# Kernel tuning notes

Measured on AMD Instinct MI355X. Metric: run time of the kernel, lower is better.

Reference implementation:

```python
import jax, jax.numpy as jnp
import numpy as np

N = 100000   # nodes
E = 1600000  # edges (avg degree 16)
D = 64       # hidden_dim == in_channels
EPS = 1e-15  # PyG DGI epsilon


def gcn_conv(x, W, b, row, col, n):
    h = x @ W                                                    # [n, D]
    deg = jax.ops.segment_sum(jnp.ones(row.shape[0], x.dtype), col,
                              num_segments=n) + 1.0              # +1 for self-loop
    dis = jax.lax.rsqrt(deg)                                     # deg^-1/2
    norm = dis[row] * dis[col]                                   # [E]
    agg = jax.ops.segment_sum(h[row] * norm[:, None], col, num_segments=n)
    return agg + h * (dis * dis)[:, None] + b                    # self-loop term + bias


def encode(x, row, col, W1, b1, W2, b2, n):
    h = jax.nn.relu(gcn_conv(x, W1, b1, row, col, n))
    return gcn_conv(h, W2, b2, row, col, n)


def setup_inputs() -> dict:
    key = jax.random.key(0)
    k = jax.random.split(key, 8)
    s = 1.0 / np.sqrt(D)
    return {
        "x": jax.random.normal(k[0], (N, D), jnp.float32),
        "W1": jax.random.uniform(k[1], (D, D), jnp.float32, -s, s),
        "b1": jnp.zeros((D,), jnp.float32),
        "W2": jax.random.uniform(k[2], (D, D), jnp.float32, -s, s),
        "b2": jnp.zeros((D,), jnp.float32),
        "W_dgi": jax.random.uniform(k[3], (D, D), jnp.float32, -s, s),
        "edge_index": jax.random.randint(k[4], (2, E), 0, N, jnp.int32),
        "perm": jax.random.permutation(k[5], N).astype(jnp.int32),
    }


def reference(x, W1, b1, W2, b2, W_dgi, edge_index, perm):
    row, col = edge_index[0], edge_index[1]
    pos_z = encode(x, row, col, W1, b1, W2, b2, N)          # [N, D]
    neg_z = encode(x[perm], row, col, W1, b1, W2, b2, N)    # corrupted features, same graph
    summary = jax.nn.sigmoid(pos_z.mean(axis=0))            # [D]
    ws = W_dgi @ summary                                    # [D]
    pos_p = jax.nn.sigmoid(pos_z @ ws)                      # [N]
    neg_p = jax.nn.sigmoid(neg_z @ ws)                      # [N]
    pos_loss = -jnp.log(pos_p + EPS).mean()
    neg_loss = -jnp.log(1.0 - neg_p + EPS).mean()
    return pos_loss + neg_loss
```

## Files before the change

kernel.cpp:

```cpp
#include <hip/hip_runtime.h>
#include <hip/hip_bf16.h>
#include <math.h>

#define GG 2048
#define RB 32
#define NB_SHIFT 9
#define NPB 512
#define BINCAP 10240
#define BINREGION 12288
#define PCHUNK 2048

typedef __hip_bfloat16 bf16;
typedef unsigned int uint;
typedef unsigned short ushort;
typedef unsigned char uchar;
typedef short bf16x8 __attribute__((ext_vector_type(8)));
typedef float f32x4 __attribute__((ext_vector_type(4)));
typedef float f32x2 __attribute__((ext_vector_type(2)));

__device__ __forceinline__ bf16  f2b(float x) { return __float2bfloat16(x); }
__device__ __forceinline__ short f2bs(float x) {
    bf16 b = __float2bfloat16(x);
    return *reinterpret_cast<short*>(&b);
}
__device__ __forceinline__ ushort packfp8(float p, float n) {
    return (ushort)__builtin_amdgcn_cvt_pk_fp8_f32(p, n, 0, false);
}
__device__ __forceinline__ f32x2 unpackfp8(uint u) {
    return __builtin_amdgcn_cvt_pk_f32_fp8((int)u, false);
}
__device__ __forceinline__ f32x2 unpackfp8_hi(uint u) {
    return __builtin_amdgcn_cvt_pk_f32_fp8((int)u, true);
}

__global__ void zero_kernel(int* __restrict__ bincnt, float* __restrict__ lossacc,
                            int nb) {
    int i = threadIdx.x;
    if (i < nb) bincnt[i] = 0;
    if (i < 2)  lossacc[i] = 0.f;
}

__global__ __launch_bounds__(256) void partition_edges(
        const int* __restrict__ row, const int* __restrict__ col,
        uint* __restrict__ bins, int* __restrict__ bincnt, int E, int nb) {
    __shared__ int lcnt[256];
    __shared__ int lbase[256];
    for (int chunk = blockIdx.x * PCHUNK; chunk < E; chunk += gridDim.x * PCHUNK) {
        int end = chunk + PCHUNK < E ? chunk + PCHUNK : E;
        if (threadIdx.x < nb) lcnt[threadIdx.x] = 0;
        __syncthreads();
        for (int e = chunk + threadIdx.x; e < end; e += 256)
            atomicAdd(&lcnt[col[e] >> NB_SHIFT], 1);
        __syncthreads();
        if (threadIdx.x < nb) {
            lbase[threadIdx.x] = atomicAdd(&bincnt[threadIdx.x], lcnt[threadIdx.x]);
            lcnt[threadIdx.x] = 0;
        }
        __syncthreads();
        for (int e = chunk + threadIdx.x; e < end; e += 256) {
            int c = col[e], r = row[e];
            int g = c >> NB_SHIFT;
            int dst = lbase[g] + atomicAdd(&lcnt[g], 1);
            if (dst < BINCAP)
                bins[(size_t)g * BINCAP + dst] = ((uint)r << NB_SHIFT) | (uint)(c & (NPB - 1));
        }
        __syncthreads();
    }
}

__global__ __launch_bounds__(256) void place_lds(
        const uint* __restrict__ bins, const int* __restrict__ bincnt,
        int* __restrict__ bucket, int* __restrict__ off, int* __restrict__ cnt,
        int N) {
    __shared__ int lcnt[NPB];
    __shared__ int s[NPB];
    __shared__ int win[BINREGION];
    int b  = blockIdx.x;
    int lo = b << NB_SHIFT;
    int base = b * BINREGION;
    int ne = bincnt[b];
    if (ne > BINCAP) ne = BINCAP;
    const uint* be = bins + (size_t)b * BINCAP;
    for (int i = threadIdx.x; i < NPB; i += 256) lcnt[i] = 0;
    __syncthreads();
    for (int i = threadIdx.x; i < ne; i += 256)
        atomicAdd(&lcnt[be[i] & (NPB - 1)], 1);
    __syncthreads();
    int i0 = threadIdx.x, i1 = threadIdx.x + 256;
    s[i0] = (lcnt[i0] + 3) & ~3;
    s[i1] = (lcnt[i1] + 3) & ~3;
    __syncthreads();
    for (int st = 1; st < NPB; st <<= 1) {
        int v0 = i0 >= st ? s[i0 - st] : 0;
        int v1 = i1 >= st ? s[i1 - st] : 0;
        __syncthreads();
        s[i0] += v0; s[i1] += v1;
        __syncthreads();
    }
    for (int i = threadIdx.x; i < NPB; i += 256) {
        int v = lo + i;
        int pc = (lcnt[i] + 3) & ~3;
        int start = s[i] - pc;
        if (v < N) { off[v] = base + start; cnt[v] = lcnt[i]; }
        lcnt[i] = start;
    }
    __syncthreads();
    for (int i = threadIdx.x; i < ne; i += 256) {
        uint u = be[i];
        int slot = atomicAdd(&lcnt[u & (NPB - 1)], 1);
        if (slot < BINREGION) win[slot] = (int)(u >> NB_SHIFT);
    }
    __syncthreads();
    int wsize = s[NPB - 1];
    if (wsize > BINREGION) wsize = BINREGION;
    for (int i = threadIdx.x * 4; i < wsize; i += 1024)
        *(int4*)&bucket[base + i] = *(const int4*)&win[i];
}

__global__ __launch_bounds__(256) void gemm1_mfma(
        const float* __restrict__ X, const float* __restrict__ W,
        const int* __restrict__ perm, const int* __restrict__ cnt,
        ushort* __restrict__ out, int n) {
    int lane = threadIdx.x & 63, wid = threadIdx.x >> 6;
    int l15 = lane & 15, lg = lane >> 4;
    bf16x8 bfr[2][4];
#pragma unroll
    for (int kt = 0; kt < 2; kt++)
#pragma unroll
        for (int nt = 0; nt < 4; nt++)
#pragma unroll
            for (int i = 0; i < 8; i++)
                bfr[kt][nt][i] = f2bs(W[(kt * 32 + lg * 8 + i) * 64 + nt * 16 + l15]);
    int ntiles = (n + 15) >> 4;
    for (int t = blockIdx.x * 4 + wid; t < ntiles; t += gridDim.x * 4) {
        int rowA = t * 16 + l15;
        if (rowA >= n) rowA = n - 1;
        int prow = perm[rowA];
        const float4* xp = (const float4*)(X + (size_t)rowA * 64);
        const float4* xn = (const float4*)(X + (size_t)prow * 64);
        bf16x8 ap[2], an[2];
#pragma unroll
        for (int kt = 0; kt < 2; kt++) {
            float4 p0 = xp[kt * 8 + lg * 2], p1 = xp[kt * 8 + lg * 2 + 1];
            float4 n0 = xn[kt * 8 + lg * 2], n1 = xn[kt * 8 + lg * 2 + 1];
            ap[kt][0] = f2bs(p0.x); ap[kt][1] = f2bs(p0.y);
            ap[kt][2] = f2bs(p0.z); ap[kt][3] = f2bs(p0.w);
            ap[kt][4] = f2bs(p1.x); ap[kt][5] = f2bs(p1.y);
            ap[kt][6] = f2bs(p1.z); ap[kt][7] = f2bs(p1.w);
            an[kt][0] = f2bs(n0.x); an[kt][1] = f2bs(n0.y);
            an[kt][2] = f2bs(n0.z); an[kt][3] = f2bs(n0.w);
            an[kt][4] = f2bs(n1.x); an[kt][5] = f2bs(n1.y);
            an[kt][6] = f2bs(n1.z); an[kt][7] = f2bs(n1.w);
        }
        f32x4 accp[4], accn[4];
#pragma unroll
        for (int nt = 0; nt < 4; nt++) { accp[nt] = (f32x4)0.f; accn[nt] = (f32x4)0.f; }
#pragma unroll
        for (int nt = 0; nt < 4; nt++) {
            accp[nt] = __builtin_amdgcn_mfma_f32_16x16x32_bf16(ap[0], bfr[0][nt], accp[nt], 0, 0, 0);
            accp[nt] = __builtin_amdgcn_mfma_f32_16x16x32_bf16(ap[1], bfr[1][nt], accp[nt], 0, 0, 0);
            accn[nt] = __builtin_amdgcn_mfma_f32_16x16x32_bf16(an[0], bfr[0][nt], accn[nt], 0, 0, 0);
            accn[nt] = __builtin_amdgcn_mfma_f32_16x16x32_bf16(an[1], bfr[1][nt], accn[nt], 0, 0, 0);
        }
        float dvr[4];
#pragma unroll
        for (int reg = 0; reg < 4; reg++) {
            int node = t * 16 + lg * 4 + reg;
            dvr[reg] = node < n ? rsqrtf((float)cnt[node] + 1.0f) : 0.f;
        }
#pragma unroll
        for (int nt = 0; nt < 4; nt++)
#pragma unroll
            for (int reg = 0; reg < 4; reg++) {
                int node = t * 16 + lg * 4 + reg;
                if (node < n)
                    out[(size_t)node * 64 + nt * 16 + l15] =
                        packfp8(accp[nt][reg] * dvr[reg], accn[nt][reg] * dvr[reg]);
            }
    }
}

__global__ __launch_bounds__(256) void gemm2_mfma(
        const ushort* __restrict__ H, const float* __restrict__ W,
        const int* __restrict__ cnt, ushort* __restrict__ out, int n) {
    int lane = threadIdx.x & 63, wid = threadIdx.x >> 6;
    int l15 = lane & 15, lg = lane >> 4;
    bf16x8 bfr[2][4];
#pragma unroll
    for (int kt = 0; kt < 2; kt++)
#pragma unroll
        for (int nt = 0; nt < 4; nt++)
#pragma unroll
            for (int i = 0; i < 8; i++)
                bfr[kt][nt][i] = f2bs(W[(kt * 32 + lg * 8 + i) * 64 + nt * 16 + l15]);
    int ntiles = (n + 15) >> 4;
    for (int t = blockIdx.x * 4 + wid; t < ntiles; t += gridDim.x * 4) {
        int rowA = t * 16 + l15;
        if (rowA >= n) rowA = n - 1;
        const uint4* h = (const uint4*)(H + (size_t)rowA * 64);
        bf16x8 ap[2], an[2];
#pragma unroll
        for (int kt = 0; kt < 2; kt++) {
            uint4 hh = h[kt * 4 + lg];
            uint uu[4] = {hh.x, hh.y, hh.z, hh.w};
#pragma unroll
            for (int j = 0; j < 4; j++) {
                f32x2 lo = unpackfp8(uu[j]);
                f32x2 hi = unpackfp8_hi(uu[j]);
                ap[kt][2 * j]     = f2bs(lo.x); an[kt][2 * j]     = f2bs(lo.y);
                ap[kt][2 * j + 1] = f2bs(hi.x); an[kt][2 * j + 1] = f2bs(hi.y);
            }
        }
        f32x4 accp[4], accn[4];
#pragma unroll
        for (int nt = 0; nt < 4; nt++) { accp[nt] = (f32x4)0.f; accn[nt] = (f32x4)0.f; }
#pragma unroll
        for (int nt = 0; nt < 4; nt++) {
            accp[nt] = __builtin_amdgcn_mfma_f32_16x16x32_bf16(ap[0], bfr[0][nt], accp[nt], 0, 0, 0);
            accp[nt] = __builtin_amdgcn_mfma_f32_16x16x32_bf16(ap[1], bfr[1][nt], accp[nt], 0, 0, 0);
            accn[nt] = __builtin_amdgcn_mfma_f32_16x16x32_bf16(an[0], bfr[0][nt], accn[nt], 0, 0, 0);
            accn[nt] = __builtin_amdgcn_mfma_f32_16x16x32_bf16(an[1], bfr[1][nt], accn[nt], 0, 0, 0);
        }
        float dvr[4];
#pragma unroll
        for (int reg = 0; reg < 4; reg++) {
            int node = t * 16 + lg * 4 + reg;
            dvr[reg] = node < n ? rsqrtf((float)cnt[node] + 1.0f) : 0.f;
        }
#pragma unroll
        for (int nt = 0; nt < 4; nt++)
#pragma unroll
            for (int reg = 0; reg < 4; reg++) {
                int node = t * 16 + lg * 4 + reg;
                if (node < n)
                    out[(size_t)node * 64 + nt * 16 + l15] =
                        packfp8(accp[nt][reg] * dvr[reg], accn[nt][reg] * dvr[reg]);
            }
    }
}

template <int MODE>
__global__ __launch_bounds__(256) void conv_packed(
        const ushort* __restrict__ g, const int* __restrict__ bucket,
        const int* __restrict__ off, const int* __restrict__ cnt,
        const float* __restrict__ bias,
        ushort* __restrict__ out, float* __restrict__ colpart, int n) {
    int lane = threadIdx.x & 63, wid = threadIdx.x >> 6;
    const uchar* gb = (const uchar*)g;
    uint l2 = (uint)lane * 2;
    __shared__ float s[256];
    float colp  = 0.f;
    float blane = bias[lane];
    int wstart = blockIdx.x * 4 + wid, wstride = gridDim.x * 4;
    for (int v = wstart; v < n; v += wstride) {
        int vu  = __builtin_amdgcn_readfirstlane(v);
        int c   = cnt[vu];
        int ofs = off[vu];
        float dv = rsqrtf((float)c + 1.0f);
        f32x2 acc0 = unpackfp8(*(const ushort*)(gb + ((size_t)(uint)vu << 7) + l2));
        f32x2 acc1 = {0.f, 0.f}, acc2 = {0.f, 0.f}, acc3 = {0.f, 0.f};
        f32x2 acc4 = {0.f, 0.f}, acc5 = {0.f, 0.f}, acc6 = {0.f, 0.f}, acc7 = {0.f, 0.f};
        const int*  bk  = bucket + ofs;
        const int4* bk4 = (const int4*)bk;
        int nq16 = c >> 4;
        for (int q = 0; q < nq16; q++) {
            int4 ra = bk4[4 * q],     rb = bk4[4 * q + 1];
            int4 rc = bk4[4 * q + 2], rd = bk4[4 * q + 3];
            uint u0  = *(const ushort*)(gb + ((size_t)(uint)ra.x << 7) + l2);
            uint u1  = *(const ushort*)(gb + ((size_t)(uint)ra.y << 7) + l2);
            uint u2  = *(const ushort*)(gb + ((size_t)(uint)ra.z << 7) + l2);
            uint u3  = *(const ushort*)(gb + ((size_t)(uint)ra.w << 7) + l2);
            uint u4  = *(const ushort*)(gb + ((size_t)(uint)rb.x << 7) + l2);
            uint u5  = *(const ushort*)(gb + ((size_t)(uint)rb.y << 7) + l2);
            uint u6  = *(const ushort*)(gb + ((size_t)(uint)rb.z << 7) + l2);
            uint u7  = *(const ushort*)(gb + ((size_t)(uint)rb.w << 7) + l2);
            uint u8  = *(const ushort*)(gb + ((size_t)(uint)rc.x << 7) + l2);
            uint u9  = *(const ushort*)(gb + ((size_t)(uint)rc.y << 7) + l2);
            uint u10 = *(const ushort*)(gb + ((size_t)(uint)rc.z << 7) + l2);
            uint u11 = *(const ushort*)(gb + ((size_t)(uint)rc.w << 7) + l2);
            uint u12 = *(const ushort*)(gb + ((size_t)(uint)rd.x << 7) + l2);
            uint u13 = *(const ushort*)(gb + ((size_t)(uint)rd.y << 7) + l2);
            uint u14 = *(const ushort*)(gb + ((size_t)(uint)rd.z << 7) + l2);
            uint u15 = *(const ushort*)(gb + ((size_t)(uint)rd.w << 7) + l2);
            acc0 += unpackfp8(u0);  acc1 += unpackfp8(u1);
            acc2 += unpackfp8(u2);  acc3 += unpackfp8(u3);
            acc4 += unpackfp8(u4);  acc5 += unpackfp8(u5);
            acc6 += unpackfp8(u6);  acc7 += unpackfp8(u7);
            acc0 += unpackfp8(u8);  acc1 += unpackfp8(u9);
            acc2 += unpackfp8(u10); acc3 += unpackfp8(u11);
            acc4 += unpackfp8(u12); acc5 += unpackfp8(u13);
            acc6 += unpackfp8(u14); acc7 += unpackfp8(u15);
        }
        int i = nq16 << 4;
        for (; i + 4 <= c; i += 4) {
            int4 r = *(const int4*)(bk + i);
            acc0 += unpackfp8(*(const ushort*)(gb + ((size_t)(uint)r.x << 7) + l2));
            acc1 += unpackfp8(*(const ushort*)(gb + ((size_t)(uint)r.y << 7) + l2));
            acc2 += unpackfp8(*(const ushort*)(gb + ((size_t)(uint)r.z << 7) + l2));
            acc3 += unpackfp8(*(const ushort*)(gb + ((size_t)(uint)r.w << 7) + l2));
        }
        for (; i < c; i++) {
            int r = bk[i];
            acc0 += unpackfp8(*(const ushort*)(gb + ((size_t)(uint)r << 7) + l2));
        }
        f32x2 acc = ((acc0 + acc1) + (acc2 + acc3)) + ((acc4 + acc5) + (acc6 + acc7));
        float rp = fmaf(dv, acc.x, blane);
        float rn = fmaf(dv, acc.y, blane);
        size_t vo = (size_t)vu * 64 + lane;
        if (MODE == 0) {
            out[vo] = packfp8(fmaxf(rp, 0.f), fmaxf(rn, 0.f));
        } else {
            out[vo] = packfp8(rp, rn);
            colp += rp;
        }
    }
    if (MODE == 1) {
        s[wid * 64 + lane] = colp;
        __syncthreads();
        if (wid == 0) {
            float t = s[lane] + s[64 + lane] + s[128 + lane] + s[192 + lane];
            colpart[(size_t)blockIdx.x * 64 + lane] = t;
        }
    }
}

__global__ __launch_bounds__(256) void colreduce_kernel(
        const float* __restrict__ colpart, float* __restrict__ colpart2) {
    int lane = threadIdx.x & 63, w = threadIdx.x >> 6;
    __shared__ float s4[4][64];
    float t = 0.f;
    int base = blockIdx.x * RB;
    for (int g = w; g < RB; g += 4) t += colpart[(size_t)(base + g) * 64 + lane];
    s4[w][lane] = t;
    __syncthreads();
    if (w == 0)
        colpart2[(size_t)blockIdx.x * 64 + lane] =
            s4[0][lane] + s4[1][lane] + s4[2][lane] + s4[3][lane];
}

__global__ void summary_kernel(const float* __restrict__ colpart,
                               const float* __restrict__ Wdgi,
                               float* __restrict__ wsv, int G, float invN) {
    __shared__ float sm[64];
    __shared__ float s4[4][64];
    int lane = threadIdx.x & 63, w = threadIdx.x >> 6;
    float t = 0.f;
    for (int g = w; g < G; g += 4) t += colpart[(size_t)g * 64 + lane];
    s4[w][lane] = t;
    __syncthreads();
    if (w == 0) {
        t = s4[0][lane] + s4[1][lane] + s4[2][lane] + s4[3][lane];
        sm[lane] = 1.f / (1.f + expf(-t * invN));
    }
    __syncthreads();
    if (threadIdx.x < 64) {
        float a = 0.f;
        for (int j = 0; j < 64; j++) a += Wdgi[threadIdx.x * 64 + j] * sm[j];
        wsv[threadIdx.x] = a;
    }
}

__global__ __launch_bounds__(256) void loss4_kernel(
        const ushort* __restrict__ z, const float* __restrict__ wsv,
        float* __restrict__ lossacc, int n) {
    int lane = threadIdx.x & 63, wid = threadIdx.x >> 6;
    int sub = lane >> 4, dch = lane & 15;
    __shared__ float s[16];
    float w0 = wsv[dch * 4], w1 = wsv[dch * 4 + 1];
    float w2 = wsv[dch * 4 + 2], w3 = wsv[dch * 4 + 3];
    float lp = 0.f, ln = 0.f;
    int nq = (n + 3) >> 2;
    for (int qi = blockIdx.x * 4 + wid; qi < nq; qi += gridDim.x * 4) {
        int v = qi * 4 + sub;
        float p = 0.f, q = 0.f;
        if (v < n) {
            uint2 u = *(const uint2*)(z + (size_t)v * 64 + dch * 4);
            f32x2 a0 = unpackfp8(u.x), a1 = unpackfp8_hi(u.x);
            f32x2 a2 = unpackfp8(u.y), a3 = unpackfp8_hi(u.y);
            p = a0.x * w0 + a1.x * w1 + a2.x * w2 + a3.x * w3;
            q = a0.y * w0 + a1.y * w1 + a2.y * w2 + a3.y * w3;
        }
        for (int o = 1; o < 16; o <<= 1) {
            p += __shfl_xor(p, o, 64);
            q += __shfl_xor(q, o, 64);
        }
        if (dch == 0 && v < n) {
            lp += -logf(1.f / (1.f + expf(-p)) + 1e-15f);
            ln += -logf(1.f / (1.f + expf( q)) + 1e-15f);
        }
    }
    lp += __shfl_xor(lp, 16, 64); ln += __shfl_xor(ln, 16, 64);
    lp += __shfl_xor(lp, 32, 64); ln += __shfl_xor(ln, 32, 64);
    if (lane == 0) { s[wid] = lp; s[8 + wid] = ln; }
    __syncthreads();
    if (threadIdx.x == 0) atomicAdd(&lossacc[0], s[0] + s[1] + s[2] + s[3]);
    if (threadIdx.x == 1) atomicAdd(&lossacc[1], s[8] + s[9] + s[10] + s[11]);
}

__global__ void finalize_kernel(const float* __restrict__ lossacc,
                                float* __restrict__ out, float invN) {
    out[0] = (lossacc[0] + lossacc[1]) * invN;
}

extern "C" void kernel_launch(void* const* d_in, const int* in_sizes, int n_in,
                              void* d_out, int out_size, void* d_ws, size_t ws_size,
                              hipStream_t stream) {
    const float* x    = (const float*)d_in[0];
    const float* W1   = (const float*)d_in[1];
    const float* b1   = (const float*)d_in[2];
    const float* W2   = (const float*)d_in[3];
    const float* b2   = (const float*)d_in[4];
    const float* Wdgi = (const float*)d_in[5];
    const int*   edge = (const int*)d_in[6];
    const int*   perm = (const int*)d_in[7];

    const int N = in_sizes[7];
    const int E = in_sizes[6] / 2;
    const int* row = edge;
    const int* col = edge + E;
    const int nb = (N + NPB - 1) >> NB_SHIFT;

    char* wsb = (char*)d_ws;
    size_t woff = 0;
    auto alloc = [&](size_t bytes) -> void* {
        void* p = wsb + woff;
        woff = (woff + bytes + 255) & ~(size_t)255;
        return p;
    };
    int*    bucket   = (int*)  alloc((size_t)nb * BINREGION * 4);
    uint*   bins     = (uint*) alloc((size_t)nb * BINCAP * 4);
    int*    bincnt   = (int*)  alloc((size_t)nb * 4);
    int*    cnt      = (int*)  alloc((size_t)N * 4);
    int*    off      = (int*)  alloc((size_t)N * 4);
    ushort* G        = (ushort*)alloc((size_t)N * 64 * 2);
    ushort* H        = (ushort*)alloc((size_t)N * 64 * 2);
    float*  colpart  = (float*)alloc((size_t)GG * 64 * 4);
    float*  colpart2 = (float*)alloc((size_t)(GG / RB) * 64 * 4);
    float*  wsv      = (float*)alloc(64 * 4);
    float*  lossacc  = (float*)alloc(2 * 4);

    zero_kernel<<<1, 256, 0, stream>>>(bincnt, lossacc, nb);

    const int nchunks = (E + PCHUNK - 1) / PCHUNK;
    partition_edges<<<nchunks, 256, 0, stream>>>(row, col, bins, bincnt, E, nb);
    place_lds<<<nb, 256, 0, stream>>>(bins, bincnt, bucket, off, cnt, N);

    gemm1_mfma<<<1024, 256, 0, stream>>>(x, W1, perm, cnt, G, N);
    conv_packed<0><<<GG, 256, 0, stream>>>(G, bucket, off, cnt, b1, H, nullptr, N);
    gemm2_mfma<<<1024, 256, 0, stream>>>(H, W2, cnt, G, N);
    conv_packed<1><<<GG, 256, 0, stream>>>(G, bucket, off, cnt, b2, H, colpart, N);

    colreduce_kernel<<<GG / RB, 256, 0, stream>>>(colpart, colpart2);
    summary_kernel<<<1, 256, 0, stream>>>(colpart2, Wdgi, wsv, GG / RB, 1.0f / N);
    loss4_kernel<<<1024, 256, 0, stream>>>(H, wsv, lossacc, N);
    finalize_kernel<<<1, 1, 0, stream>>>(lossacc, (float*)d_out, 1.0f / N);
}
```

Measured before the change: 198.7 us.

## Fuse first conv aggregation with second GEMM and merge tail kernels via last-block pattern

The first-layer gather/aggregate (conv_packed<0>) is fused into the second GEMM. Each wave aggregates 16 nodes, stages the ReLU'd rows as bf16 in LDS and feeds them straight into MFMA, so the intermediate H never goes to global memory in fp8. The column reduction and summary kernels are merged using an atomic ticket so the last block finishes the summary. The finalize kernel is folded into the loss kernel the same way. This removes several launches and one global round-trip, and H now stays in bf16, which changes precision slightly. The cost is that each wave aggregates its 16 nodes serially before the MFMA, and the grid size is fixed at 1568 blocks.

```diff
diff --git a/kernel.cpp b/kernel.cpp
--- a/kernel.cpp
+++ b/kernel.cpp
@@ -23,6 +23,12 @@
     bf16 b = __float2bfloat16(x);
     return *reinterpret_cast<short*>(&b);
 }
+__device__ __forceinline__ uint packbf(float p, float n) {
+    bf16 bp = f2b(p), bn = f2b(n);
+    ushort up = *reinterpret_cast<ushort*>(&bp);
+    ushort un = *reinterpret_cast<ushort*>(&bn);
+    return (uint)up | ((uint)un << 16);
+}
 __device__ __forceinline__ ushort packfp8(float p, float n) {
     return (ushort)__builtin_amdgcn_cvt_pk_fp8_f32(p, n, 0, false);
 }
@@ -34,10 +40,10 @@
 }
 
 __global__ void zero_kernel(int* __restrict__ bincnt, float* __restrict__ lossacc,
-                            int nb) {
+                            int* __restrict__ flags, int nb) {
     int i = threadIdx.x;
     if (i < nb) bincnt[i] = 0;
-    if (i < 2)  lossacc[i] = 0.f;
+    if (i < 2) { lossacc[i] = 0.f; flags[i] = 0; }
 }
 
 __global__ __launch_bounds__(256) void partition_edges(
@@ -180,11 +186,17 @@
     }
 }
 
-__global__ __launch_bounds__(256) void gemm2_mfma(
-        const ushort* __restrict__ H, const float* __restrict__ W,
-        const int* __restrict__ cnt, ushort* __restrict__ out, int n) {
+__global__ __launch_bounds__(256) void convgemm_kernel(
+        const ushort* __restrict__ g, const int* __restrict__ bucket,
+        const int* __restrict__ off, const int* __restrict__ cnt,
+        const float* __restrict__ bias, const float* __restrict__ W,
+        ushort* __restrict__ out, int n) {
     int lane = threadIdx.x & 63, wid = threadIdx.x >> 6;
     int l15 = lane & 15, lg = lane >> 4;
+    const uchar* gb = (const uchar*)g;
+    uint l2 = (uint)lane * 2;
+    __shared__ uint hrow[4][16][65];
+    float blane = bias[lane];
     bf16x8 bfr[2][4];
 #pragma unroll
     for (int kt = 0; kt < 2; kt++)
@@ -195,22 +207,74 @@
                 bfr[kt][nt][i] = f2bs(W[(kt * 32 + lg * 8 + i) * 64 + nt * 16 + l15]);
     int ntiles = (n + 15) >> 4;
     for (int t = blockIdx.x * 4 + wid; t < ntiles; t += gridDim.x * 4) {
-        int rowA = t * 16 + l15;
-        if (rowA >= n) rowA = n - 1;
-        const uint4* h = (const uint4*)(H + (size_t)rowA * 64);
+        int base = t << 4;
+        for (int j = 0; j < 16; j++) {
+            int v = base + j;
+            if (v >= n) v = n - 1;
+            int vu  = __builtin_amdgcn_readfirstlane(v);
+            int c   = cnt[vu];
+            int ofs = off[vu];
+            float dv = rsqrtf((float)c + 1.0f);
+            f32x2 acc0 = unpackfp8(*(const ushort*)(gb + ((size_t)(uint)vu << 7) + l2));
+            f32x2 acc1 = {0.f, 0.f}, acc2 = {0.f, 0.f}, acc3 = {0.f, 0.f};
+            f32x2 acc4 = {0.f, 0.f}, acc5 = {0.f, 0.f}, acc6 = {0.f, 0.f}, acc7 = {0.f, 0.f};
+            const int*  bk  = bucket + ofs;
+            const int4* bk4 = (const int4*)bk;
+            int nq16 = c >> 4;
+            for (int q = 0; q < nq16; q++) {
+                int4 ra = bk4[4 * q],     rb = bk4[4 * q + 1];
+                int4 rc = bk4[4 * q + 2], rd = bk4[4 * q + 3];
+                uint u0  = *(const ushort*)(gb + ((size_t)(uint)ra.x << 7) + l2);
+                uint u1  = *(const ushort*)(gb + ((size_t)(uint)ra.y << 7) + l2);
+                uint u2  = *(const ushort*)(gb + ((size_t)(uint)ra.z << 7) + l2);
+                uint u3  = *(const ushort*)(gb + ((size_t)(uint)ra.w << 7) + l2);
+                uint u4  = *(const ushort*)(gb + ((size_t)(uint)rb.x << 7) + l2);
+                uint u5  = *(const ushort*)(gb + ((size_t)(uint)rb.y << 7) + l2);
+                uint u6  = *(const ushort*)(gb + ((size_t)(uint)rb.z << 7) + l2);
+                uint u7  = *(const ushort*)(gb + ((size_t)(uint)rb.w << 7) + l2);
+                uint u8  = *(const ushort*)(gb + ((size_t)(uint)rc.x << 7) + l2);
+                uint u9  = *(const ushort*)(gb + ((size_t)(uint)rc.y << 7) + l2);
+                uint u10 = *(const ushort*)(gb + ((size_t)(uint)rc.z << 7) + l2);
+                uint u11 = *(const ushort*)(gb + ((size_t)(uint)rc.w << 7) + l2);
+                uint u12 = *(const ushort*)(gb + ((size_t)(uint)rd.x << 7) + l2);
+                uint u13 = *(const ushort*)(gb + ((size_t)(uint)rd.y << 7) + l2);
+                uint u14 = *(const ushort*)(gb + ((size_t)(uint)rd.z << 7) + l2);
+                uint u15 = *(const ushort*)(gb + ((size_t)(uint)rd.w << 7) + l2);
+                acc0 += unpackfp8(u0);  acc1 += unpackfp8(u1);
+                acc2 += unpackfp8(u2);  acc3 += unpackfp8(u3);
+                acc4 += unpackfp8(u4);  acc5 += unpackfp8(u5);
+                acc6 += unpackfp8(u6);  acc7 += unpackfp8(u7);
+                acc0 += unpackfp8(u8);  acc1 += unpackfp8(u9);
+                acc2 += unpackfp8(u10); acc3 += unpackfp8(u11);
+                acc4 += unpackfp8(u12); acc5 += unpackfp8(u13);
+                acc6 += unpackfp8(u14); acc7 += unpackfp8(u15);
+            }
+            int i = nq16 << 4;
+            for (; i + 4 <= c; i += 4) {
+                int4 r = *(const int4*)(bk + i);
+                acc0 += unpackfp8(*(const ushort*)(gb + ((size_t)(uint)r.x << 7) + l2));
+                acc1 += unpackfp8(*(const ushort*)(gb + ((size_t)(uint)r.y << 7) + l2));
+                acc2 += unpackfp8(*(const ushort*)(gb + ((size_t)(uint)r.z << 7) + l2));
+                acc3 += unpackfp8(*(const ushort*)(gb + ((size_t)(uint)r.w << 7) + l2));
+            }
+            for (; i < c; i++) {
+                int r = bk[i];
+                acc0 += unpackfp8(*(const ushort*)(gb + ((size_t)(uint)r << 7) + l2));
+            }
+            f32x2 acc = ((acc0 + acc1) + (acc2 + acc3)) + ((acc4 + acc5) + (acc6 + acc7));
+            float rp = fmaf(dv, acc.x, blane);
+            float rn = fmaf(dv, acc.y, blane);
+            hrow[wid][j][lane] = packbf(fmaxf(rp, 0.f), fmaxf(rn, 0.f));
+        }
         bf16x8 ap[2], an[2];
 #pragma unroll
-        for (int kt = 0; kt < 2; kt++) {
-            uint4 hh = h[kt * 4 + lg];
-            uint uu[4] = {hh.x, hh.y, hh.z, hh.w};
-#pragma unroll
-            for (int j = 0; j < 4; j++) {
-                f32x2 lo = unpackfp8(uu[j]);
-                f32x2 hi = unpackfp8_hi(uu[j]);
-                ap[kt][2 * j]     = f2bs(lo.x); an[kt][2 * j]     = f2bs(lo.y);
-                ap[kt][2 * j + 1] = f2bs(hi.x); an[kt][2 * j + 1] = f2bs(hi.y);
+        for (int kt = 0; kt < 2; kt++)
+#pragma unroll
+            for (int i = 0; i < 8; i++) {
+                uint u = hrow[wid][l15][kt * 32 + lg * 8 + i];
+                ap[kt][i] = (short)(u & 0xFFFFu);
+                an[kt][i] = (short)(u >> 16);
             }
-        }
         f32x4 accp[4], accn[4];
 #pragma unroll
         for (int nt = 0; nt < 4; nt++) { accp[nt] = (f32x4)0.f; accn[nt] = (f32x4)0.f; }
@@ -224,14 +288,14 @@
         float dvr[4];
 #pragma unroll
         for (int reg = 0; reg < 4; reg++) {
-            int node = t * 16 + lg * 4 + reg;
+            int node = base + lg * 4 + reg;
             dvr[reg] = node < n ? rsqrtf((float)cnt[node] + 1.0f) : 0.f;
         }
 #pragma unroll
         for (int nt = 0; nt < 4; nt++)
 #pragma unroll
             for (int reg = 0; reg < 4; reg++) {
-                int node = t * 16 + lg * 4 + reg;
+                int node = base + lg * 4 + reg;
                 if (node < n)
                     out[(size_t)node * 64 + nt * 16 + l15] =
                         packfp8(accp[nt][reg] * dvr[reg], accn[nt][reg] * dvr[reg]);
@@ -239,7 +303,6 @@
     }
 }
 
-template <int MODE>
 __global__ __launch_bounds__(256) void conv_packed(
         const ushort* __restrict__ g, const int* __restrict__ bucket,
         const int* __restrict__ off, const int* __restrict__ cnt,
@@ -306,28 +369,24 @@
         f32x2 acc = ((acc0 + acc1) + (acc2 + acc3)) + ((acc4 + acc5) + (acc6 + acc7));
         float rp = fmaf(dv, acc.x, blane);
         float rn = fmaf(dv, acc.y, blane);
-        size_t vo = (size_t)vu * 64 + lane;
-        if (MODE == 0) {
-            out[vo] = packfp8(fmaxf(rp, 0.f), fmaxf(rn, 0.f));
-        } else {
-            out[vo] = packfp8(rp, rn);
-            colp += rp;
-        }
-    }
-    if (MODE == 1) {
-        s[wid * 64 + lane] = colp;
-        __syncthreads();
-        if (wid == 0) {
-            float t = s[lane] + s[64 + lane] + s[128 + lane] + s[192 + lane];
-            colpart[(size_t)blockIdx.x * 64 + lane] = t;
-        }
-    }
-}
-
-__global__ __launch_bounds__(256) void colreduce_kernel(
-        const float* __restrict__ colpart, float* __restrict__ colpart2) {
+        out[(size_t)vu * 64 + lane] = packfp8(rp, rn);
+        colp += rp;
+    }
+    s[wid * 64 + lane] = colp;
+    __syncthreads();
+    if (wid == 0) {
+        float t = s[lane] + s[64 + lane] + s[128 + lane] + s[192 + lane];
+        colpart[(size_t)blockIdx.x * 64 + lane] = t;
+    }
+}
+
+__global__ __launch_bounds__(256) void colreduce_summary(
+        const float* __restrict__ colpart, float* __restrict__ colpart2,
+        const float* __restrict__ Wdgi, float* __restrict__ wsv,
+        int* __restrict__ flag, float invN) {
     int lane = threadIdx.x & 63, w = threadIdx.x >> 6;
     __shared__ float s4[4][64];
+    __shared__ int tk;
     float t = 0.f;
     int base = blockIdx.x * RB;
     for (int g = w; g < RB; g += 4) t += colpart[(size_t)(base + g) * 64 + lane];
@@ -336,36 +395,39 @@
     if (w == 0)
         colpart2[(size_t)blockIdx.x * 64 + lane] =
             s4[0][lane] + s4[1][lane] + s4[2][lane] + s4[3][lane];
-}
-
-__global__ void summary_kernel(const float* __restrict__ colpart,
-                               const float* __restrict__ Wdgi,
-                               float* __restrict__ wsv, int G, float invN) {
-    __shared__ float sm[64];
-    __shared__ float s4[4][64];
-    int lane = threadIdx.x & 63, w = threadIdx.x >> 6;
-    float t = 0.f;
-    for (int g = w; g < G; g += 4) t += colpart[(size_t)g * 64 + lane];
-    s4[w][lane] = t;
-    __syncthreads();
-    if (w == 0) {
-        t = s4[0][lane] + s4[1][lane] + s4[2][lane] + s4[3][lane];
-        sm[lane] = 1.f / (1.f + expf(-t * invN));
-    }
-    __syncthreads();
-    if (threadIdx.x < 64) {
-        float a = 0.f;
-        for (int j = 0; j < 64; j++) a += Wdgi[threadIdx.x * 64 + j] * sm[j];
-        wsv[threadIdx.x] = a;
+    __threadfence();
+    if (threadIdx.x == 0) tk = atomicAdd(flag, 1);
+    __syncthreads();
+    if (tk == (int)gridDim.x - 1) {
+        __threadfence();
+        __shared__ float sm[64];
+        __shared__ float p4[4][64];
+        float u = 0.f;
+        for (int g = w; g < (int)gridDim.x; g += 4)
+            u += colpart2[(size_t)g * 64 + lane];
+        p4[w][lane] = u;
+        __syncthreads();
+        if (w == 0) {
+            u = p4[0][lane] + p4[1][lane] + p4[2][lane] + p4[3][lane];
+            sm[lane] = 1.f / (1.f + expf(-u * invN));
+        }
+        __syncthreads();
+        if (threadIdx.x < 64) {
+            float a = 0.f;
+            for (int j = 0; j < 64; j++) a += Wdgi[threadIdx.x * 64 + j] * sm[j];
+            wsv[threadIdx.x] = a;
+        }
     }
 }
 
 __global__ __launch_bounds__(256) void loss4_kernel(
         const ushort* __restrict__ z, const float* __restrict__ wsv,
-        float* __restrict__ lossacc, int n) {
+        float* __restrict__ lossacc, int* __restrict__ flag,
+        float* __restrict__ outp, float invN, int n) {
     int lane = threadIdx.x & 63, wid = threadIdx.x >> 6;
     int sub = lane >> 4, dch = lane & 15;
     __shared__ float s[16];
+    __shared__ int tk;
     float w0 = wsv[dch * 4], w1 = wsv[dch * 4 + 1];
     float w2 = wsv[dch * 4 + 2], w3 = wsv[dch * 4 + 3];
     float lp = 0.f, ln = 0.f;
@@ -395,11 +457,15 @@
     __syncthreads();
     if (threadIdx.x == 0) atomicAdd(&lossacc[0], s[0] + s[1] + s[2] + s[3]);
     if (threadIdx.x == 1) atomicAdd(&lossacc[1], s[8] + s[9] + s[10] + s[11]);
-}
-
-__global__ void finalize_kernel(const float* __restrict__ lossacc,
-                                float* __restrict__ out, float invN) {
-    out[0] = (lossacc[0] + lossacc[1]) * invN;
+    __threadfence();
+    __syncthreads();
+    if (threadIdx.x == 0) tk = atomicAdd(flag, 1);
+    __syncthreads();
+    if (tk == (int)gridDim.x - 1 && threadIdx.x == 0) {
+        float a = atomicAdd(&lossacc[0], 0.f);
+        float b = atomicAdd(&lossacc[1], 0.f);
+        outp[0] = (a + b) * invN;
+    }
 }
 
 extern "C" void kernel_launch(void* const* d_in, const int* in_sizes, int n_in,
@@ -433,25 +499,25 @@
     int*    cnt      = (int*)  alloc((size_t)N * 4);
     int*    off      = (int*)  alloc((size_t)N * 4);
     ushort* G        = (ushort*)alloc((size_t)N * 64 * 2);
-    ushort* H        = (ushort*)alloc((size_t)N * 64 * 2);
+    ushort* G2       = (ushort*)alloc((size_t)N * 64 * 2);
     float*  colpart  = (float*)alloc((size_t)GG * 64 * 4);
     float*  colpart2 = (float*)alloc((size_t)(GG / RB) * 64 * 4);
     float*  wsv      = (float*)alloc(64 * 4);
     float*  lossacc  = (float*)alloc(2 * 4);
-
-    zero_kernel<<<1, 256, 0, stream>>>(bincnt, lossacc, nb);
+    int*    flags    = (int*)  alloc(2 * 4);
+
+    zero_kernel<<<1, 256, 0, stream>>>(bincnt, lossacc, flags, nb);
 
     const int nchunks = (E + PCHUNK - 1) / PCHUNK;
     partition_edges<<<nchunks, 256, 0, stream>>>(row, col, bins, bincnt, E, nb);
     place_lds<<<nb, 256, 0, stream>>>(bins, bincnt, bucket, off, cnt, N);
 
     gemm1_mfma<<<1024, 256, 0, stream>>>(x, W1, perm, cnt, G, N);
-    conv_packed<0><<<GG, 256, 0, stream>>>(G, bucket, off, cnt, b1, H, nullptr, N);
-    gemm2_mfma<<<1024, 256, 0, stream>>>(H, W2, cnt, G, N);
-    conv_packed<1><<<GG, 256, 0, stream>>>(G, bucket, off, cnt, b2, H, colpart, N);
-
-    colreduce_kernel<<<GG / RB, 256, 0, stream>>>(colpart, colpart2);
-    summary_kernel<<<1, 256, 0, stream>>>(colpart2, Wdgi, wsv, GG / RB, 1.0f / N);
-    loss4_kernel<<<1024, 256, 0, stream>>>(H, wsv, lossacc, N);
-    finalize_kernel<<<1, 1, 0, stream>>>(lossacc, (float*)d_out, 1.0f / N);
-}
+    convgemm_kernel<<<1568, 256, 0, stream>>>(G, bucket, off, cnt, b1, W2, G2, N);
+    conv_packed<<<GG, 256, 0, stream>>>(G2, bucket, off, cnt, b2, G, colpart, N);
+
+    colreduce_summary<<<GG / RB, 256, 0, stream>>>(colpart, colpart2, Wdgi, wsv,
+                                                   &flags[0], 1.0f / N);
+    loss4_kernel<<<1024, 256, 0, stream>>>(G, wsv, lossacc, &flags[1],
+                                           (float*)d_out, 1.0f / N, N);
+}
```

New measurement: 269.3 us. 1.36x slower.
